# Optimization experiments

Hardware: AMD Instinct MI355X
Metric: run time of the kernel (lower is better)

## Reference

```python
import jax, jax.numpy as jnp
import numpy as np

MAX_JOINTS = 143

def setup_inputs() -> dict:
    key = jax.random.key(0)
    ks = jax.random.split(key, 8)
    d_model, latent_dim, feat = 256, 512, 13
    s = lambda n: 1.0 / np.sqrt(n)
    return {
        "z": jax.random.normal(ks[0], (32, latent_dim), jnp.float32),
        "W_latent": jax.random.normal(ks[1], (latent_dim, d_model), jnp.float32) * s(latent_dim),
        "b_latent": jnp.zeros((d_model,), jnp.float32),
        "joint_emb": jax.random.normal(ks[2], (MAX_JOINTS, d_model), jnp.float32),
        "frame_emb": jax.random.normal(ks[3], (120, d_model), jnp.float32),
        "ln_gamma": jnp.ones((d_model,), jnp.float32),
        "ln_beta": jnp.zeros((d_model,), jnp.float32),
        "W1": jax.random.normal(ks[4], (d_model, d_model), jnp.float32) * s(d_model),
        "b1": jnp.zeros((d_model,), jnp.float32),
        "W2": jax.random.normal(ks[5], (d_model, feat), jnp.float32) * s(d_model),
        "b2": jnp.zeros((feat,), jnp.float32),
        "max_frames": 120,
    }

def reference(z, W_latent, b_latent, joint_emb, frame_emb, ln_gamma, ln_beta, W1, b1, W2, b2, max_frames):
    # base: [B, d]
    base = z @ W_latent + b_latent
    fe = frame_emb[:max_frames]  # [F, d]
    # three-way broadcast sum -> [B, J, F, d]
    hidden = base[:, None, None, :] + joint_emb[None, :, None, :] + fe[None, None, :, :]
    # LayerNorm over last dim (eps=1e-5, torch default)
    mu = jnp.mean(hidden, axis=-1, keepdims=True)
    var = jnp.mean(jnp.square(hidden - mu), axis=-1, keepdims=True)
    h = (hidden - mu) * jax.lax.rsqrt(var + 1e-5) * ln_gamma + ln_beta
    # MLP: Linear -> exact GELU -> Linear
    h = jax.nn.gelu(h @ W1 + b1, approximate=False)
    out = h @ W2 + b2  # [B, J, F, feat]
    return jnp.transpose(out, (0, 1, 3, 2))  # [B, J, feat, F]
```

## Files before the change

### kernel.cpp

```cpp
#include <hip/hip_runtime.h>
#include <hip/hip_bf16.h>

typedef __bf16 bf16x8 __attribute__((ext_vector_type(8)));
typedef float  f32x4  __attribute__((ext_vector_type(4)));
typedef float  f32x2  __attribute__((ext_vector_type(2)));

#define B_  32
#define J_  143
#define F_  120
#define D_  256
#define L_  512
#define C_  13
#define M_  4576
#define MP_ 4736
#define FE0 4576
#define NK  512
#define NN  384

static __device__ __forceinline__ unsigned short bits(__bf16 h) {
  return __builtin_bit_cast(unsigned short, h);
}

__device__ __forceinline__ f32x2 gelu2(f32x2 u) {
  f32x2 x2 = u * u;
  f32x2 t  = u * (x2 * -0.1029432f + -2.3022082f);
  f32x2 e;
  e.x = __builtin_amdgcn_exp2f(t.x);
  e.y = __builtin_amdgcn_exp2f(t.y);
  f32x2 d = e + 1.0f;
  f32x2 r;
  r.x = __builtin_amdgcn_rcpf(d.x);
  r.y = __builtin_amdgcn_rcpf(d.y);
  return u * r;
}

__global__ __launch_bounds__(256) void prepAll_kernel(
    const float* __restrict__ z, const float* __restrict__ Wl,
    const float* __restrict__ bl, const float* __restrict__ W1,
    const float* __restrict__ gamma, const float* __restrict__ beta,
    const float* __restrict__ b1, const float* __restrict__ frame_emb,
    const float* __restrict__ W2,
    float* __restrict__ base, unsigned short* __restrict__ BT,
    float* __restrict__ bW1, float* __restrict__ Sfe, float* __restrict__ Sfe2,
    unsigned short* __restrict__ W2T, float* __restrict__ zerov) {
  const int t = threadIdx.x, bid = blockIdx.x;
  const int lane = t & 63, wv = t >> 6;
  __shared__ float zs[L_];
  __shared__ float ra[4], rb[4];
  if (bid < 32) {
    zs[t]       = z[bid * L_ + t];
    zs[t + 256] = z[bid * L_ + t + 256];
    __syncthreads();
    float acc = 0.f;
    #pragma unroll 32
    for (int k = 0; k < L_; ++k) acc = __builtin_fmaf(zs[k], Wl[k * D_ + t], acc);
    base[bid * D_ + t] = acc + bl[t];
    return;
  }
  const int n = bid - 32;
  if (n < 256) {
    const float w1v = W1[t * D_ + n];
    float a = gamma[t] * w1v;
    float b = beta[t] * w1v;
    const float wg = a;
    #pragma unroll
    for (int m = 1; m < 64; m <<= 1) { a += __shfl_xor(a, m); b += __shfl_xor(b, m); }
    if (lane == 0) { ra[wv] = a; rb[wv] = b; }
    __syncthreads();
    const float cs = ra[0] + ra[1] + ra[2] + ra[3];
    if (t == 0) bW1[n] = rb[0] + rb[1] + rb[2] + rb[3] + b1[n];
    const float m = __builtin_fmaf(cs, -1.f / 256.f, wg);
    const __bf16 hi = (__bf16)m;
    const __bf16 lo = (__bf16)(m - (float)hi);
    BT[n * NK + t]       = bits(hi);
    BT[n * NK + 256 + t] = bits(lo);
  } else if (n < 376) {
    const int f = n - 256;
    const float v = frame_emb[f * D_ + t];
    float a = v, b = v * v;
    #pragma unroll
    for (int m = 1; m < 64; m <<= 1) { a += __shfl_xor(a, m); b += __shfl_xor(b, m); }
    if (lane == 0) { ra[wv] = a; rb[wv] = b; }
    __syncthreads();
    if (t == 0) {
      Sfe[f]  = ra[0] + ra[1] + ra[2] + ra[3];
      Sfe2[f] = rb[0] + rb[1] + rb[2] + rb[3];
    }
    const __bf16 hi = (__bf16)v;
    const __bf16 lo = (__bf16)(v - (float)hi);
    BT[n * NK + t]       = bits(hi);
    BT[n * NK + 256 + t] = bits(lo);
  } else if (n < 384) {
    BT[n * NK + t] = 0; BT[n * NK + 256 + t] = 0;
  } else if (n < 400) {
    const int c = n - 384;
    const float v = (c < C_) ? W2[t * C_ + c] : 0.f;
    W2T[c * D_ + t] = bits((__bf16)v);
  } else {
    zerov[t] = 0.f;
  }
}

__global__ __launch_bounds__(256, 4) void gemmB_kernel(
    const float* __restrict__ base, const float* __restrict__ joint,
    const float* __restrict__ fe, const float* __restrict__ zerov,
    const unsigned short* __restrict__ BT,
    float* __restrict__ PX, unsigned short* __restrict__ P2h,
    float* __restrict__ Sc, float* __restrict__ Sc2) {
  const int tid = threadIdx.x, lane = tid & 63, wave = tid >> 6;
  const int lrow = lane & 15, lgrp = lane >> 4;
  const int rb = blockIdx.x / 12, cb = blockIdx.x % 12;
  const int rowbase = rb * 64 + wave * 16;
  const int colbase = cb * 32;
  const int r = rowbase + lrow;

  const float *p1, *p2;
  if (r < M_) {
    const int b = r / J_, j = r - b * J_;
    p1 = base + b * D_; p2 = joint + j * D_;
  } else if (r < FE0 + F_) {
    p1 = fe + (r - FE0) * D_; p2 = zerov;
  } else {
    p1 = zerov; p2 = zerov;
  }

  const unsigned short* Bp = BT + (size_t)(colbase + lrow) * NK + lgrp * 8;
  f32x4 acc[2] = {};
  float ssum = 0.f, ssq = 0.f;
  #pragma unroll
  for (int s8 = 0; s8 < 8; ++s8) {
    const int k0 = s8 * 32 + lgrp * 8;
    const float4 ca = *(const float4*)(p1 + k0);
    const float4 cb4 = *(const float4*)(p1 + k0 + 4);
    const float4 da = *(const float4*)(p2 + k0);
    const float4 db = *(const float4*)(p2 + k0 + 4);
    const float c[8] = {ca.x + da.x, ca.y + da.y, ca.z + da.z, ca.w + da.w,
                        cb4.x + db.x, cb4.y + db.y, cb4.z + db.z, cb4.w + db.w};
    bf16x8 ahi, alo;
    #pragma unroll
    for (int e = 0; e < 8; ++e) {
      const __bf16 h = (__bf16)c[e];
      ahi[e] = h;
      alo[e] = (__bf16)(c[e] - (float)h);
    }
    if (cb == 0) {
      #pragma unroll
      for (int e = 0; e < 8; ++e) { ssum += c[e]; ssq = __builtin_fmaf(c[e], c[e], ssq); }
    }
    bf16x8 bhi[2], blo[2];
    #pragma unroll
    for (int nf = 0; nf < 2; ++nf) {
      bhi[nf] = *(const bf16x8*)(Bp + (size_t)nf * 16 * NK + s8 * 32);
      blo[nf] = *(const bf16x8*)(Bp + (size_t)nf * 16 * NK + 256 + s8 * 32);
    }
    #pragma unroll
    for (int nf = 0; nf < 2; ++nf) {
      acc[nf] = __builtin_amdgcn_mfma_f32_16x16x32_bf16(ahi, bhi[nf], acc[nf], 0, 0, 0);
      acc[nf] = __builtin_amdgcn_mfma_f32_16x16x32_bf16(alo, bhi[nf], acc[nf], 0, 0, 0);
      acc[nf] = __builtin_amdgcn_mfma_f32_16x16x32_bf16(ahi, blo[nf], acc[nf], 0, 0, 0);
    }
  }

  if (cb == 0) {
    ssum += __shfl_xor(ssum, 16); ssum += __shfl_xor(ssum, 32);
    ssq  += __shfl_xor(ssq, 16);  ssq  += __shfl_xor(ssq, 32);
    if (lgrp == 0) { Sc[r] = ssum; Sc2[r] = ssq; }
  }

  #pragma unroll
  for (int nf = 0; nf < 2; ++nf)
    #pragma unroll
    for (int r4 = 0; r4 < 4; ++r4) {
      const int orow = rowbase + lgrp * 4 + r4;
      const int ocol = colbase + nf * 16 + lrow;
      const float v = acc[nf][r4];
      PX[(size_t)orow * NN + ocol] = v;
      const int fr = orow - FE0;
      if (fr >= 0 && fr < F_ && ocol < 256)
        P2h[fr * 256 + ocol] = bits((__bf16)v);
    }
}

__global__ __launch_bounds__(256, 6) void mainC_kernel(
    const float* __restrict__ PX, const unsigned short* __restrict__ P2h,
    const float* __restrict__ bW1,
    const float* __restrict__ Sc, const float* __restrict__ Sc2,
    const float* __restrict__ Sfe, const float* __restrict__ Sfe2,
    const unsigned short* __restrict__ W2T, const float* __restrict__ b2,
    float* __restrict__ out) {
  __shared__ float pc[2][256], bw[256], rstdl[2][128];
  __shared__ __align__(16) unsigned short w2l[4096];
  const int tid = threadIdx.x, lane = tid & 63, wave = tid >> 6;
  const int lrow = lane & 15, lgrp = lane >> 4;
  const int bj0 = blockIdx.x * 2;

  #pragma unroll
  for (int q = 0; q < 2; ++q) pc[q][tid] = PX[(size_t)(bj0 + q) * NN + tid];
  bw[tid] = bW1[tid];
  {
    const int r = tid >> 4;
    const int b0 = tid * 32;
    const int sb = b0 ^ ((r & 7) << 4);
    *(uint4*)((char*)w2l + sb)        = *(const uint4*)((const char*)W2T + b0);
    *(uint4*)((char*)w2l + (sb ^ 16)) = *(const uint4*)((const char*)W2T + b0 + 16);
  }
  {
    const int q = tid >> 7;
    const int f = tid & 127;
    const int fc = f < F_ ? f : F_ - 1;
    const float X = PX[(size_t)(bj0 + q) * NN + 256 + fc];
    const float mu = (Sc[bj0 + q] + Sfe[fc]) * (1.f / 256.f);
    const float ms = __builtin_fmaf(2.f, X, Sc2[bj0 + q] + Sfe2[fc]) * (1.f / 256.f);
    rstdl[q][f] = rsqrtf(ms - mu * mu + 1e-5f);
  }
  __syncthreads();

  const int r0 = wave * 32 + lrow, r1 = r0 + 16;
  const int f0 = r0 < F_ ? r0 : F_ - 1;
  const int f1 = r1 < F_ ? r1 : F_ - 1;
  f32x2 RS0[2], RS1[2];
  #pragma unroll
  for (int q = 0; q < 2; ++q) {
    const float a = rstdl[q][r0], b = rstdl[q][r1];
    RS0[q].x = a; RS0[q].y = a;
    RS1[q].x = b; RS1[q].y = b;
  }
  const unsigned short* __restrict__ q0p = P2h + f0 * 256 + lgrp * 8;
  const unsigned short* __restrict__ q1p = P2h + f1 * 256 + lgrp * 8;

  bf16x8 qc0 = *(const bf16x8*)(q0p);
  bf16x8 qc1 = *(const bf16x8*)(q1p);

  f32x4 acc[2][2] = {};
  #pragma unroll
  for (int s = 0; s < 8; ++s) {
    const int n0 = s * 32 + lgrp * 8;
    bf16x8 qn0, qn1;
    if (s < 7) {
      qn0 = *(const bf16x8*)(q0p + (s + 1) * 32);
      qn1 = *(const bf16x8*)(q1p + (s + 1) * 32);
    }
    const bf16x8 w2f = *(const bf16x8*)((const char*)w2l +
        ((lrow * 512 + n0 * 2) ^ ((lrow & 7) << 4)));
    bf16x8 af[2][2];
    #pragma unroll
    for (int ep = 0; ep < 4; ++ep) {
      const int e0 = 2 * ep;
      f32x2 Q0, Q1, BV;
      Q0.x = (float)qc0[e0]; Q0.y = (float)qc0[e0 + 1];
      Q1.x = (float)qc1[e0]; Q1.y = (float)qc1[e0 + 1];
      BV = *(const f32x2*)(&bw[n0 + e0]);
      #pragma unroll
      for (int q = 0; q < 2; ++q) {
        const f32x2 P = *(const f32x2*)(&pc[q][n0 + e0]);
        const f32x2 U0 = __builtin_elementwise_fma(RS0[q], P + Q0, BV);
        const f32x2 U1 = __builtin_elementwise_fma(RS1[q], P + Q1, BV);
        const f32x2 G0 = gelu2(U0);
        const f32x2 G1 = gelu2(U1);
        af[q][0][e0] = (__bf16)G0.x; af[q][0][e0 + 1] = (__bf16)G0.y;
        af[q][1][e0] = (__bf16)G1.x; af[q][1][e0 + 1] = (__bf16)G1.y;
      }
    }
    #pragma unroll
    for (int q = 0; q < 2; ++q) {
      acc[q][0] = __builtin_amdgcn_mfma_f32_16x16x32_bf16(af[q][0], w2f, acc[q][0], 0, 0, 0);
      acc[q][1] = __builtin_amdgcn_mfma_f32_16x16x32_bf16(af[q][1], w2f, acc[q][1], 0, 0, 0);
    }
    qc0 = qn0; qc1 = qn1;
  }

  if (lrow < C_) {
    const float bias = b2[lrow];
    #pragma unroll
    for (int q = 0; q < 2; ++q)
      #pragma unroll
      for (int mf = 0; mf < 2; ++mf) {
        const int f = wave * 32 + mf * 16 + lgrp * 4;
        if (f < F_) {
          float4 v;
          v.x = acc[q][mf][0] + bias;
          v.y = acc[q][mf][1] + bias;
          v.z = acc[q][mf][2] + bias;
          v.w = acc[q][mf][3] + bias;
          *(float4*)(out + (size_t)(bj0 + q) * (C_ * F_) + lrow * F_ + f) = v;
        }
      }
  }
}

extern "C" void kernel_launch(void* const* d_in, const int* in_sizes, int n_in,
                              void* d_out, int out_size, void* d_ws, size_t ws_size,
                              hipStream_t stream) {
  const float* z         = (const float*)d_in[0];
  const float* W_latent  = (const float*)d_in[1];
  const float* b_latent  = (const float*)d_in[2];
  const float* joint_emb = (const float*)d_in[3];
  const float* frame_emb = (const float*)d_in[4];
  const float* ln_g      = (const float*)d_in[5];
  const float* ln_b      = (const float*)d_in[6];
  const float* W1        = (const float*)d_in[7];
  const float* b1        = (const float*)d_in[8];
  const float* W2        = (const float*)d_in[9];
  const float* b2        = (const float*)d_in[10];
  float* out = (float*)d_out;

  char* ws = (char*)d_ws;
  float*          base  = (float*)(ws + 0);
  unsigned short* W2T   = (unsigned short*)(ws + 32768);
  float*          bW1   = (float*)(ws + 40960);
  float*          Sfe   = (float*)(ws + 41984);
  float*          Sfe2  = (float*)(ws + 42496);
  float*          Sc    = (float*)(ws + 43008);
  float*          Sc2   = (float*)(ws + 61952);
  float*          zerov = (float*)(ws + 80896);
  unsigned short* BT    = (unsigned short*)(ws + 81920);
  unsigned short* P2h   = (unsigned short*)(ws + 700416);
  float*          PX    = (float*)(ws + 8388608);

  prepAll_kernel<<<433, 256, 0, stream>>>(z, W_latent, b_latent, W1, ln_g, ln_b, b1,
                                          frame_emb, W2, base, BT, bW1, Sfe, Sfe2,
                                          W2T, zerov);
  gemmB_kernel<<<888, 256, 0, stream>>>(base, joint_emb, frame_emb, zerov, BT,
                                        PX, P2h, Sc, Sc2);
  mainC_kernel<<<M_ / 2, 256, 0, stream>>>(PX, P2h, bW1, Sc, Sc2, Sfe, Sfe2, W2T, b2, out);
}
```

Measured before the change: 85.62 us.

## Fuse three kernels into one cooperative persistent kernel with grid syncs

Merges the prep, projection GEMM and MLP kernels into one cooperative kernel of 763 blocks that separates phases with grid-wide syncs. The phase-3 loop iterates persistently over (b,j) pairs. The GEMM tile is widened to 64 columns per block, and the bf16 P2h copy is dropped so the frame projections are read as fp32 from PX. The goal is to remove launch gaps between kernels, at the cost of grid-sync overhead, lower occupancy (3 blocks per CU) and wider fp32 loads in the inner loop. A non-cooperative three-launch fallback is kept.

```diff
diff --git a/kernel.cpp b/kernel.cpp
--- a/kernel.cpp
+++ b/kernel.cpp
@@ -1,5 +1,8 @@
 #include <hip/hip_runtime.h>
 #include <hip/hip_bf16.h>
+#include <hip/hip_cooperative_groups.h>
+
+namespace cg = cooperative_groups;
 
 typedef __bf16 bf16x8 __attribute__((ext_vector_type(8)));
 typedef float  f32x4  __attribute__((ext_vector_type(4)));
@@ -16,6 +19,8 @@
 #define FE0 4576
 #define NK  512
 #define NN  384
+#define GRID_  763
+#define PAIRS_ 2288
 
 static __device__ __forceinline__ unsigned short bits(__bf16 h) {
   return __builtin_bit_cast(unsigned short, h);
@@ -34,274 +39,277 @@
   return u * r;
 }
 
-__global__ __launch_bounds__(256) void prepAll_kernel(
+__global__ __launch_bounds__(256, 3) void fused_kernel(
+    int phase,
     const float* __restrict__ z, const float* __restrict__ Wl,
-    const float* __restrict__ bl, const float* __restrict__ W1,
-    const float* __restrict__ gamma, const float* __restrict__ beta,
-    const float* __restrict__ b1, const float* __restrict__ frame_emb,
-    const float* __restrict__ W2,
+    const float* __restrict__ bl, const float* __restrict__ joint,
+    const float* __restrict__ fe, const float* __restrict__ gamma,
+    const float* __restrict__ beta, const float* __restrict__ W1,
+    const float* __restrict__ b1, const float* __restrict__ W2,
+    const float* __restrict__ b2,
     float* __restrict__ base, unsigned short* __restrict__ BT,
     float* __restrict__ bW1, float* __restrict__ Sfe, float* __restrict__ Sfe2,
-    unsigned short* __restrict__ W2T, float* __restrict__ zerov) {
-  const int t = threadIdx.x, bid = blockIdx.x;
-  const int lane = t & 63, wv = t >> 6;
+    unsigned short* __restrict__ W2T, float* __restrict__ zerov,
+    float* __restrict__ PX, float* __restrict__ Sc, float* __restrict__ Sc2,
+    float* __restrict__ out) {
   __shared__ float zs[L_];
   __shared__ float ra[4], rb[4];
-  if (bid < 32) {
-    zs[t]       = z[bid * L_ + t];
-    zs[t + 256] = z[bid * L_ + t + 256];
-    __syncthreads();
-    float acc = 0.f;
-    #pragma unroll 32
-    for (int k = 0; k < L_; ++k) acc = __builtin_fmaf(zs[k], Wl[k * D_ + t], acc);
-    base[bid * D_ + t] = acc + bl[t];
-    return;
-  }
-  const int n = bid - 32;
-  if (n < 256) {
-    const float w1v = W1[t * D_ + n];
-    float a = gamma[t] * w1v;
-    float b = beta[t] * w1v;
-    const float wg = a;
-    #pragma unroll
-    for (int m = 1; m < 64; m <<= 1) { a += __shfl_xor(a, m); b += __shfl_xor(b, m); }
-    if (lane == 0) { ra[wv] = a; rb[wv] = b; }
-    __syncthreads();
-    const float cs = ra[0] + ra[1] + ra[2] + ra[3];
-    if (t == 0) bW1[n] = rb[0] + rb[1] + rb[2] + rb[3] + b1[n];
-    const float m = __builtin_fmaf(cs, -1.f / 256.f, wg);
-    const __bf16 hi = (__bf16)m;
-    const __bf16 lo = (__bf16)(m - (float)hi);
-    BT[n * NK + t]       = bits(hi);
-    BT[n * NK + 256 + t] = bits(lo);
-  } else if (n < 376) {
-    const int f = n - 256;
-    const float v = frame_emb[f * D_ + t];
-    float a = v, b = v * v;
-    #pragma unroll
-    for (int m = 1; m < 64; m <<= 1) { a += __shfl_xor(a, m); b += __shfl_xor(b, m); }
-    if (lane == 0) { ra[wv] = a; rb[wv] = b; }
-    __syncthreads();
-    if (t == 0) {
-      Sfe[f]  = ra[0] + ra[1] + ra[2] + ra[3];
-      Sfe2[f] = rb[0] + rb[1] + rb[2] + rb[3];
-    }
-    const __bf16 hi = (__bf16)v;
-    const __bf16 lo = (__bf16)(v - (float)hi);
-    BT[n * NK + t]       = bits(hi);
-    BT[n * NK + 256 + t] = bits(lo);
-  } else if (n < 384) {
-    BT[n * NK + t] = 0; BT[n * NK + 256 + t] = 0;
-  } else if (n < 400) {
-    const int c = n - 384;
-    const float v = (c < C_) ? W2[t * C_ + c] : 0.f;
-    W2T[c * D_ + t] = bits((__bf16)v);
-  } else {
-    zerov[t] = 0.f;
-  }
-}
-
-__global__ __launch_bounds__(256, 4) void gemmB_kernel(
-    const float* __restrict__ base, const float* __restrict__ joint,
-    const float* __restrict__ fe, const float* __restrict__ zerov,
-    const unsigned short* __restrict__ BT,
-    float* __restrict__ PX, unsigned short* __restrict__ P2h,
-    float* __restrict__ Sc, float* __restrict__ Sc2) {
-  const int tid = threadIdx.x, lane = tid & 63, wave = tid >> 6;
-  const int lrow = lane & 15, lgrp = lane >> 4;
-  const int rb = blockIdx.x / 12, cb = blockIdx.x % 12;
-  const int rowbase = rb * 64 + wave * 16;
-  const int colbase = cb * 32;
-  const int r = rowbase + lrow;
-
-  const float *p1, *p2;
-  if (r < M_) {
-    const int b = r / J_, j = r - b * J_;
-    p1 = base + b * D_; p2 = joint + j * D_;
-  } else if (r < FE0 + F_) {
-    p1 = fe + (r - FE0) * D_; p2 = zerov;
-  } else {
-    p1 = zerov; p2 = zerov;
-  }
-
-  const unsigned short* Bp = BT + (size_t)(colbase + lrow) * NK + lgrp * 8;
-  f32x4 acc[2] = {};
-  float ssum = 0.f, ssq = 0.f;
-  #pragma unroll
-  for (int s8 = 0; s8 < 8; ++s8) {
-    const int k0 = s8 * 32 + lgrp * 8;
-    const float4 ca = *(const float4*)(p1 + k0);
-    const float4 cb4 = *(const float4*)(p1 + k0 + 4);
-    const float4 da = *(const float4*)(p2 + k0);
-    const float4 db = *(const float4*)(p2 + k0 + 4);
-    const float c[8] = {ca.x + da.x, ca.y + da.y, ca.z + da.z, ca.w + da.w,
-                        cb4.x + db.x, cb4.y + db.y, cb4.z + db.z, cb4.w + db.w};
-    bf16x8 ahi, alo;
-    #pragma unroll
-    for (int e = 0; e < 8; ++e) {
-      const __bf16 h = (__bf16)c[e];
-      ahi[e] = h;
-      alo[e] = (__bf16)(c[e] - (float)h);
-    }
-    if (cb == 0) {
-      #pragma unroll
-      for (int e = 0; e < 8; ++e) { ssum += c[e]; ssq = __builtin_fmaf(c[e], c[e], ssq); }
-    }
-    bf16x8 bhi[2], blo[2];
-    #pragma unroll
-    for (int nf = 0; nf < 2; ++nf) {
-      bhi[nf] = *(const bf16x8*)(Bp + (size_t)nf * 16 * NK + s8 * 32);
-      blo[nf] = *(const bf16x8*)(Bp + (size_t)nf * 16 * NK + 256 + s8 * 32);
-    }
-    #pragma unroll
-    for (int nf = 0; nf < 2; ++nf) {
-      acc[nf] = __builtin_amdgcn_mfma_f32_16x16x32_bf16(ahi, bhi[nf], acc[nf], 0, 0, 0);
-      acc[nf] = __builtin_amdgcn_mfma_f32_16x16x32_bf16(alo, bhi[nf], acc[nf], 0, 0, 0);
-      acc[nf] = __builtin_amdgcn_mfma_f32_16x16x32_bf16(ahi, blo[nf], acc[nf], 0, 0, 0);
-    }
-  }
-
-  if (cb == 0) {
-    ssum += __shfl_xor(ssum, 16); ssum += __shfl_xor(ssum, 32);
-    ssq  += __shfl_xor(ssq, 16);  ssq  += __shfl_xor(ssq, 32);
-    if (lgrp == 0) { Sc[r] = ssum; Sc2[r] = ssq; }
-  }
-
-  #pragma unroll
-  for (int nf = 0; nf < 2; ++nf)
-    #pragma unroll
-    for (int r4 = 0; r4 < 4; ++r4) {
-      const int orow = rowbase + lgrp * 4 + r4;
-      const int ocol = colbase + nf * 16 + lrow;
-      const float v = acc[nf][r4];
-      PX[(size_t)orow * NN + ocol] = v;
-      const int fr = orow - FE0;
-      if (fr >= 0 && fr < F_ && ocol < 256)
-        P2h[fr * 256 + ocol] = bits((__bf16)v);
-    }
-}
-
-__global__ __launch_bounds__(256, 6) void mainC_kernel(
-    const float* __restrict__ PX, const unsigned short* __restrict__ P2h,
-    const float* __restrict__ bW1,
-    const float* __restrict__ Sc, const float* __restrict__ Sc2,
-    const float* __restrict__ Sfe, const float* __restrict__ Sfe2,
-    const unsigned short* __restrict__ W2T, const float* __restrict__ b2,
-    float* __restrict__ out) {
   __shared__ float pc[2][256], bw[256], rstdl[2][128];
   __shared__ __align__(16) unsigned short w2l[4096];
-  const int tid = threadIdx.x, lane = tid & 63, wave = tid >> 6;
+
+  const int tid  = threadIdx.x;
+  const int lane = tid & 63, wv = tid >> 6;
   const int lrow = lane & 15, lgrp = lane >> 4;
-  const int bj0 = blockIdx.x * 2;
-
-  #pragma unroll
-  for (int q = 0; q < 2; ++q) pc[q][tid] = PX[(size_t)(bj0 + q) * NN + tid];
-  bw[tid] = bW1[tid];
-  {
-    const int r = tid >> 4;
-    const int b0 = tid * 32;
-    const int sb = b0 ^ ((r & 7) << 4);
-    *(uint4*)((char*)w2l + sb)        = *(const uint4*)((const char*)W2T + b0);
-    *(uint4*)((char*)w2l + (sb ^ 16)) = *(const uint4*)((const char*)W2T + b0 + 16);
+  const int bid  = blockIdx.x;
+  const bool coop = (phase == 0);
+
+  if (coop || phase == 1) {
+    if (bid < 32) {
+      zs[tid]       = z[bid * L_ + tid];
+      zs[tid + 256] = z[bid * L_ + tid + 256];
+      __syncthreads();
+      float acc = 0.f;
+      #pragma unroll 32
+      for (int k = 0; k < L_; ++k) acc = __builtin_fmaf(zs[k], Wl[k * D_ + tid], acc);
+      base[bid * D_ + tid] = acc + bl[tid];
+    } else if (bid < 433) {
+      const int n = bid - 32;
+      if (n < 256) {
+        const float w1v = W1[tid * D_ + n];
+        float a = gamma[tid] * w1v;
+        float b = beta[tid] * w1v;
+        const float wg = a;
+        #pragma unroll
+        for (int m = 1; m < 64; m <<= 1) { a += __shfl_xor(a, m); b += __shfl_xor(b, m); }
+        if (lane == 0) { ra[wv] = a; rb[wv] = b; }
+        __syncthreads();
+        const float cs = ra[0] + ra[1] + ra[2] + ra[3];
+        if (tid == 0) bW1[n] = rb[0] + rb[1] + rb[2] + rb[3] + b1[n];
+        const float m = __builtin_fmaf(cs, -1.f / 256.f, wg);
+        const __bf16 hi = (__bf16)m;
+        const __bf16 lo = (__bf16)(m - (float)hi);
+        BT[n * NK + tid]       = bits(hi);
+        BT[n * NK + 256 + tid] = bits(lo);
+      } else if (n < 376) {
+        const int f = n - 256;
+        const float v = fe[f * D_ + tid];
+        float a = v, b = v * v;
+        #pragma unroll
+        for (int m = 1; m < 64; m <<= 1) { a += __shfl_xor(a, m); b += __shfl_xor(b, m); }
+        if (lane == 0) { ra[wv] = a; rb[wv] = b; }
+        __syncthreads();
+        if (tid == 0) {
+          Sfe[f]  = ra[0] + ra[1] + ra[2] + ra[3];
+          Sfe2[f] = rb[0] + rb[1] + rb[2] + rb[3];
+        }
+        const __bf16 hi = (__bf16)v;
+        const __bf16 lo = (__bf16)(v - (float)hi);
+        BT[n * NK + tid]       = bits(hi);
+        BT[n * NK + 256 + tid] = bits(lo);
+      } else if (n < 384) {
+        BT[n * NK + tid] = 0; BT[n * NK + 256 + tid] = 0;
+      } else if (n < 400) {
+        const int c = n - 384;
+        const float v = (c < C_) ? W2[tid * C_ + c] : 0.f;
+        W2T[c * D_ + tid] = bits((__bf16)v);
+      } else {
+        zerov[tid] = 0.f;
+      }
+    }
   }
-  {
-    const int q = tid >> 7;
-    const int f = tid & 127;
-    const int fc = f < F_ ? f : F_ - 1;
-    const float X = PX[(size_t)(bj0 + q) * NN + 256 + fc];
-    const float mu = (Sc[bj0 + q] + Sfe[fc]) * (1.f / 256.f);
-    const float ms = __builtin_fmaf(2.f, X, Sc2[bj0 + q] + Sfe2[fc]) * (1.f / 256.f);
-    rstdl[q][f] = rsqrtf(ms - mu * mu + 1e-5f);
+  if (coop) cg::this_grid().sync();
+
+  if ((coop || phase == 2) && bid < 444) {
+    const int rb_ = bid / 6, cb_ = bid % 6;
+    const int rowbase = rb_ * 64 + wv * 16;
+    const int colbase = cb_ * 64;
+    const int r = rowbase + lrow;
+
+    const float *p1, *p2;
+    if (r < M_) {
+      const int b = r / J_, j = r - b * J_;
+      p1 = base + b * D_; p2 = joint + j * D_;
+    } else if (r < FE0 + F_) {
+      p1 = fe + (r - FE0) * D_; p2 = zerov;
+    } else {
+      p1 = zerov; p2 = zerov;
+    }
+
+    const unsigned short* Bp = BT + (size_t)(colbase + lrow) * NK + lgrp * 8;
+    f32x4 acc[4] = {};
+    float ssum = 0.f, ssq = 0.f;
+    #pragma unroll
+    for (int s8 = 0; s8 < 8; ++s8) {
+      const int k0 = s8 * 32 + lgrp * 8;
+      const float4 ca = *(const float4*)(p1 + k0);
+      const float4 cb4 = *(const float4*)(p1 + k0 + 4);
+      const float4 da = *(const float4*)(p2 + k0);
+      const float4 db = *(const float4*)(p2 + k0 + 4);
+      const float c[8] = {ca.x + da.x, ca.y + da.y, ca.z + da.z, ca.w + da.w,
+                          cb4.x + db.x, cb4.y + db.y, cb4.z + db.z, cb4.w + db.w};
+      bf16x8 ahi, alo;
+      #pragma unroll
+      for (int e = 0; e < 8; ++e) {
+        const __bf16 h = (__bf16)c[e];
+        ahi[e] = h;
+        alo[e] = (__bf16)(c[e] - (float)h);
+      }
+      if (cb_ == 0) {
+        #pragma unroll
+        for (int e = 0; e < 8; ++e) { ssum += c[e]; ssq = __builtin_fmaf(c[e], c[e], ssq); }
+      }
+      bf16x8 bhi[4], blo[4];
+      #pragma unroll
+      for (int nf = 0; nf < 4; ++nf) {
+        bhi[nf] = *(const bf16x8*)(Bp + (size_t)nf * 16 * NK + s8 * 32);
+        blo[nf] = *(const bf16x8*)(Bp + (size_t)nf * 16 * NK + 256 + s8 * 32);
+      }
+      #pragma unroll
+      for (int nf = 0; nf < 4; ++nf)
+        acc[nf] = __builtin_amdgcn_mfma_f32_16x16x32_bf16(ahi, bhi[nf], acc[nf], 0, 0, 0);
+      #pragma unroll
+      for (int nf = 0; nf < 4; ++nf)
+        acc[nf] = __builtin_amdgcn_mfma_f32_16x16x32_bf16(alo, bhi[nf], acc[nf], 0, 0, 0);
+      #pragma unroll
+      for (int nf = 0; nf < 4; ++nf)
+        acc[nf] = __builtin_amdgcn_mfma_f32_16x16x32_bf16(ahi, blo[nf], acc[nf], 0, 0, 0);
+    }
+
+    if (cb_ == 0) {
+      ssum += __shfl_xor(ssum, 16); ssum += __shfl_xor(ssum, 32);
+      ssq  += __shfl_xor(ssq, 16);  ssq  += __shfl_xor(ssq, 32);
+      if (lgrp == 0) { Sc[r] = ssum; Sc2[r] = ssq; }
+    }
+
+    #pragma unroll
+    for (int nf = 0; nf < 4; ++nf)
+      #pragma unroll
+      for (int r4 = 0; r4 < 4; ++r4)
+        PX[(size_t)(rowbase + lgrp * 4 + r4) * NN + colbase + nf * 16 + lrow] = acc[nf][r4];
   }
-  __syncthreads();
-
-  const int r0 = wave * 32 + lrow, r1 = r0 + 16;
-  const int f0 = r0 < F_ ? r0 : F_ - 1;
-  const int f1 = r1 < F_ ? r1 : F_ - 1;
-  f32x2 RS0[2], RS1[2];
-  #pragma unroll
-  for (int q = 0; q < 2; ++q) {
-    const float a = rstdl[q][r0], b = rstdl[q][r1];
-    RS0[q].x = a; RS0[q].y = a;
-    RS1[q].x = b; RS1[q].y = b;
-  }
-  const unsigned short* __restrict__ q0p = P2h + f0 * 256 + lgrp * 8;
-  const unsigned short* __restrict__ q1p = P2h + f1 * 256 + lgrp * 8;
-
-  bf16x8 qc0 = *(const bf16x8*)(q0p);
-  bf16x8 qc1 = *(const bf16x8*)(q1p);
-
-  f32x4 acc[2][2] = {};
-  #pragma unroll
-  for (int s = 0; s < 8; ++s) {
-    const int n0 = s * 32 + lgrp * 8;
-    bf16x8 qn0, qn1;
-    if (s < 7) {
-      qn0 = *(const bf16x8*)(q0p + (s + 1) * 32);
-      qn1 = *(const bf16x8*)(q1p + (s + 1) * 32);
-    }
-    const bf16x8 w2f = *(const bf16x8*)((const char*)w2l +
-        ((lrow * 512 + n0 * 2) ^ ((lrow & 7) << 4)));
-    bf16x8 af[2][2];
-    #pragma unroll
-    for (int ep = 0; ep < 4; ++ep) {
-      const int e0 = 2 * ep;
-      f32x2 Q0, Q1, BV;
-      Q0.x = (float)qc0[e0]; Q0.y = (float)qc0[e0 + 1];
-      Q1.x = (float)qc1[e0]; Q1.y = (float)qc1[e0 + 1];
-      BV = *(const f32x2*)(&bw[n0 + e0]);
+  if (coop) cg::this_grid().sync();
+
+  if (coop || phase == 3) {
+    bw[tid] = bW1[tid];
+    {
+      const int rr = tid >> 4;
+      const int b0 = tid * 32;
+      const int sb = b0 ^ ((rr & 7) << 4);
+      *(uint4*)((char*)w2l + sb)        = *(const uint4*)((const char*)W2T + b0);
+      *(uint4*)((char*)w2l + (sb ^ 16)) = *(const uint4*)((const char*)W2T + b0 + 16);
+    }
+    const float bias = (lrow < C_) ? b2[lrow] : 0.f;
+
+    const int r0 = wv * 32 + lrow, r1 = r0 + 16;
+    const int f0 = r0 < F_ ? r0 : F_ - 1;
+    const int f1 = r1 < F_ ? r1 : F_ - 1;
+    const float* __restrict__ q0p = PX + (size_t)(FE0 + f0) * NN + lgrp * 8;
+    const float* __restrict__ q1p = PX + (size_t)(FE0 + f1) * NN + lgrp * 8;
+
+    for (int pair = bid; pair < PAIRS_; pair += (int)gridDim.x) {
+      const int bj0 = pair * 2;
+      __syncthreads();
+
+      #pragma unroll
+      for (int q = 0; q < 2; ++q) pc[q][tid] = PX[(size_t)(bj0 + q) * NN + tid];
+      {
+        const int q = tid >> 7;
+        const int f = tid & 127;
+        const int fc = f < F_ ? f : F_ - 1;
+        const float X = PX[(size_t)(bj0 + q) * NN + 256 + fc];
+        const float mu = (Sc[bj0 + q] + Sfe[fc]) * (1.f / 256.f);
+        const float ms = __builtin_fmaf(2.f, X, Sc2[bj0 + q] + Sfe2[fc]) * (1.f / 256.f);
+        rstdl[q][f] = rsqrtf(ms - mu * mu + 1e-5f);
+      }
+      __syncthreads();
+
+      f32x2 RS0[2], RS1[2];
       #pragma unroll
       for (int q = 0; q < 2; ++q) {
-        const f32x2 P = *(const f32x2*)(&pc[q][n0 + e0]);
-        const f32x2 U0 = __builtin_elementwise_fma(RS0[q], P + Q0, BV);
-        const f32x2 U1 = __builtin_elementwise_fma(RS1[q], P + Q1, BV);
-        const f32x2 G0 = gelu2(U0);
-        const f32x2 G1 = gelu2(U1);
-        af[q][0][e0] = (__bf16)G0.x; af[q][0][e0 + 1] = (__bf16)G0.y;
-        af[q][1][e0] = (__bf16)G1.x; af[q][1][e0 + 1] = (__bf16)G1.y;
-      }
-    }
-    #pragma unroll
-    for (int q = 0; q < 2; ++q) {
-      acc[q][0] = __builtin_amdgcn_mfma_f32_16x16x32_bf16(af[q][0], w2f, acc[q][0], 0, 0, 0);
-      acc[q][1] = __builtin_amdgcn_mfma_f32_16x16x32_bf16(af[q][1], w2f, acc[q][1], 0, 0, 0);
-    }
-    qc0 = qn0; qc1 = qn1;
-  }
-
-  if (lrow < C_) {
-    const float bias = b2[lrow];
-    #pragma unroll
-    for (int q = 0; q < 2; ++q)
-      #pragma unroll
-      for (int mf = 0; mf < 2; ++mf) {
-        const int f = wave * 32 + mf * 16 + lgrp * 4;
-        if (f < F_) {
-          float4 v;
-          v.x = acc[q][mf][0] + bias;
-          v.y = acc[q][mf][1] + bias;
-          v.z = acc[q][mf][2] + bias;
-          v.w = acc[q][mf][3] + bias;
-          *(float4*)(out + (size_t)(bj0 + q) * (C_ * F_) + lrow * F_ + f) = v;
+        const float a = rstdl[q][r0], b = rstdl[q][r1];
+        RS0[q].x = a; RS0[q].y = a;
+        RS1[q].x = b; RS1[q].y = b;
+      }
+
+      float4 qa0 = *(const float4*)(q0p), qa1 = *(const float4*)(q0p + 4);
+      float4 qb0 = *(const float4*)(q1p), qb1 = *(const float4*)(q1p + 4);
+
+      f32x4 acc[2][2] = {};
+      #pragma unroll
+      for (int s = 0; s < 8; ++s) {
+        const int n0 = s * 32 + lgrp * 8;
+        float4 na0, na1, nb0, nb1;
+        if (s < 7) {
+          na0 = *(const float4*)(q0p + (s + 1) * 32);
+          na1 = *(const float4*)(q0p + (s + 1) * 32 + 4);
+          nb0 = *(const float4*)(q1p + (s + 1) * 32);
+          nb1 = *(const float4*)(q1p + (s + 1) * 32 + 4);
         }
-      }
+        const bf16x8 w2f = *(const bf16x8*)((const char*)w2l +
+            ((lrow * 512 + n0 * 2) ^ ((lrow & 7) << 4)));
+        const float q0v[8] = {qa0.x, qa0.y, qa0.z, qa0.w, qa1.x, qa1.y, qa1.z, qa1.w};
+        const float q1v[8] = {qb0.x, qb0.y, qb0.z, qb0.w, qb1.x, qb1.y, qb1.z, qb1.w};
+        bf16x8 af[2][2];
+        #pragma unroll
+        for (int ep = 0; ep < 4; ++ep) {
+          const int e0 = 2 * ep;
+          f32x2 Q0, Q1, BV;
+          Q0.x = q0v[e0]; Q0.y = q0v[e0 + 1];
+          Q1.x = q1v[e0]; Q1.y = q1v[e0 + 1];
+          BV = *(const f32x2*)(&bw[n0 + e0]);
+          #pragma unroll
+          for (int q = 0; q < 2; ++q) {
+            const f32x2 P = *(const f32x2*)(&pc[q][n0 + e0]);
+            const f32x2 U0 = __builtin_elementwise_fma(RS0[q], P + Q0, BV);
+            const f32x2 U1 = __builtin_elementwise_fma(RS1[q], P + Q1, BV);
+            const f32x2 G0 = gelu2(U0);
+            const f32x2 G1 = gelu2(U1);
+            af[q][0][e0] = (__bf16)G0.x; af[q][0][e0 + 1] = (__bf16)G0.y;
+            af[q][1][e0] = (__bf16)G1.x; af[q][1][e0 + 1] = (__bf16)G1.y;
+          }
+        }
+        #pragma unroll
+        for (int q = 0; q < 2; ++q) {
+          acc[q][0] = __builtin_amdgcn_mfma_f32_16x16x32_bf16(af[q][0], w2f, acc[q][0], 0, 0, 0);
+          acc[q][1] = __builtin_amdgcn_mfma_f32_16x16x32_bf16(af[q][1], w2f, acc[q][1], 0, 0, 0);
+        }
+        qa0 = na0; qa1 = na1; qb0 = nb0; qb1 = nb1;
+      }
+
+      if (lrow < C_) {
+        #pragma unroll
+        for (int q = 0; q < 2; ++q)
+          #pragma unroll
+          for (int mf = 0; mf < 2; ++mf) {
+            const int f = wv * 32 + mf * 16 + lgrp * 4;
+            if (f < F_) {
+              float4 v;
+              v.x = acc[q][mf][0] + bias;
+              v.y = acc[q][mf][1] + bias;
+              v.z = acc[q][mf][2] + bias;
+              v.w = acc[q][mf][3] + bias;
+              *(float4*)(out + (size_t)(bj0 + q) * (C_ * F_) + lrow * F_ + f) = v;
+            }
+          }
+      }
+    }
   }
 }
 
 extern "C" void kernel_launch(void* const* d_in, const int* in_sizes, int n_in,
                               void* d_out, int out_size, void* d_ws, size_t ws_size,
                               hipStream_t stream) {
-  const float* z         = (const float*)d_in[0];
-  const float* W_latent  = (const float*)d_in[1];
-  const float* b_latent  = (const float*)d_in[2];
-  const float* joint_emb = (const float*)d_in[3];
-  const float* frame_emb = (const float*)d_in[4];
-  const float* ln_g      = (const float*)d_in[5];
-  const float* ln_b      = (const float*)d_in[6];
-  const float* W1        = (const float*)d_in[7];
-  const float* b1        = (const float*)d_in[8];
-  const float* W2        = (const float*)d_in[9];
-  const float* b2        = (const float*)d_in[10];
+  const float* z     = (const float*)d_in[0];
+  const float* Wl    = (const float*)d_in[1];
+  const float* bl    = (const float*)d_in[2];
+  const float* joint = (const float*)d_in[3];
+  const float* fe    = (const float*)d_in[4];
+  const float* gamma = (const float*)d_in[5];
+  const float* beta  = (const float*)d_in[6];
+  const float* W1    = (const float*)d_in[7];
+  const float* b1    = (const float*)d_in[8];
+  const float* W2    = (const float*)d_in[9];
+  const float* b2    = (const float*)d_in[10];
   float* out = (float*)d_out;
 
   char* ws = (char*)d_ws;
@@ -314,13 +322,30 @@
   float*          Sc2   = (float*)(ws + 61952);
   float*          zerov = (float*)(ws + 80896);
   unsigned short* BT    = (unsigned short*)(ws + 81920);
-  unsigned short* P2h   = (unsigned short*)(ws + 700416);
   float*          PX    = (float*)(ws + 8388608);
 
-  prepAll_kernel<<<433, 256, 0, stream>>>(z, W_latent, b_latent, W1, ln_g, ln_b, b1,
-                                          frame_emb, W2, base, BT, bW1, Sfe, Sfe2,
-                                          W2T, zerov);
-  gemmB_kernel<<<888, 256, 0, stream>>>(base, joint_emb, frame_emb, zerov, BT,
-                                        PX, P2h, Sc, Sc2);
-  mainC_kernel<<<M_ / 2, 256, 0, stream>>>(PX, P2h, bW1, Sc, Sc2, Sfe, Sfe2, W2T, b2, out);
+  int phase0 = 0;
+  void* args[] = {
+    (void*)&phase0,
+    (void*)&z, (void*)&Wl, (void*)&bl, (void*)&joint, (void*)&fe,
+    (void*)&gamma, (void*)&beta, (void*)&W1, (void*)&b1, (void*)&W2, (void*)&b2,
+    (void*)&base, (void*)&BT, (void*)&bW1, (void*)&Sfe, (void*)&Sfe2,
+    (void*)&W2T, (void*)&zerov, (void*)&PX, (void*)&Sc, (void*)&Sc2, (void*)&out
+  };
+
+  int maxB = 0;
+  hipError_t qe = hipOccupancyMaxActiveBlocksPerMultiprocessor(&maxB, fused_kernel, 256, 0);
+  const bool coopOK = (qe == hipSuccess) && (maxB >= 3);
+
+  if (coopOK) {
+    hipLaunchCooperativeKernel((const void*)fused_kernel, dim3(GRID_), dim3(256),
+                               args, 0, stream);
+  } else {
+    fused_kernel<<<433, 256, 0, stream>>>(1, z, Wl, bl, joint, fe, gamma, beta, W1,
+        b1, W2, b2, base, BT, bW1, Sfe, Sfe2, W2T, zerov, PX, Sc, Sc2, out);
+    fused_kernel<<<444, 256, 0, stream>>>(2, z, Wl, bl, joint, fe, gamma, beta, W1,
+        b1, W2, b2, base, BT, bW1, Sfe, Sfe2, W2T, zerov, PX, Sc, Sc2, out);
+    fused_kernel<<<PAIRS_, 256, 0, stream>>>(3, z, Wl, bl, joint, fe, gamma, beta, W1,
+        b1, W2, b2, base, BT, bW1, Sfe, Sfe2, W2T, zerov, PX, Sc, Sc2, out);
+  }
 }
```

Result: faster. 83.86 us (-2.1%).
